# Kernel optimization log

Hardware: AMD Instinct MI355X
Metric: run time of the kernel (lower is better)

The kernel has to match this reference:

```python
import jax, jax.numpy as jnp
import numpy as np

B, S, D = 1, 2048, 2048
H, DH, DHID, DKER = 16, 128, 128, 64
EPS = 1e-6

def _gelu(x):
    return jax.nn.gelu(x, approximate=False)  # torch F.gelu default is exact erf

def setup_inputs() -> dict:
    key = jax.random.key(0)
    ks = jax.random.split(key, 12)
    inp = {
        'q': jax.random.normal(ks[0], (B, S, D), jnp.float32),
        'k': jax.random.normal(ks[1], (B, S, D), jnp.float32),
        'v': jax.random.normal(ks[2], (B, S, D), jnp.float32),
        'lr_attn_mask': jax.random.randint(ks[3], (1, 1, S, S), 0, 2) > 0,
        'sparse_norms_lse': jax.random.normal(ks[4], (B, H, S, 1), jnp.float32),
        'sparse_attn_weights': jax.random.normal(ks[5], (B, H, S, S), jnp.float32) * 0.1,
        'kernel_q_mat1': jax.random.normal(ks[6], (H, DH, DHID), jnp.float32) * 0.05,
        'kernel_k_mat1': jax.random.normal(ks[7], (H, DH, DHID), jnp.float32) * 0.05,
        'kernel_q_mat2': jax.random.normal(ks[8], (H, DHID, DKER), jnp.float32) * 0.05,
        'kernel_k_mat2': jax.random.normal(ks[9], (H, DHID, DKER), jnp.float32) * 0.05,
        'interaction_k': jax.random.normal(ks[10], (H, DKER, DKER), jnp.float32) * 0.05,
        'scalingD': jnp.ones((1, H, 1, DKER), jnp.float32) * 1e-4,
        'scalingD2': jnp.ones((1, H, 1, DKER), jnp.float32) * 1e-4,
    }
    return inp

def reference(q, k, v, lr_attn_mask, sparse_norms_lse, sparse_attn_weights,
              kernel_q_mat1, kernel_k_mat1, kernel_q_mat2, kernel_k_mat2,
              interaction_k, scalingD, scalingD2):
    b, s, d = q.shape
    dh = d // H
    # [B,S,D] -> [B,H,S,dh]
    q = q.reshape(b, s, H, dh).transpose(0, 2, 1, 3)
    k = k.reshape(b, s, H, dh).transpose(0, 2, 1, 3)
    v = v.reshape(b, s, H, dh).transpose(0, 2, 1, 3)
    # per-head kernel feature maps (dropout is identity, p=0.0)
    q = _gelu(jnp.einsum('bhsd,hde->bhse', q, kernel_q_mat1))
    q = _gelu(jnp.einsum('bhsd,hde->bhse', q, kernel_q_mat2))
    k = _gelu(jnp.einsum('bhsd,hde->bhse', k, kernel_k_mat1))
    k = jnp.abs(scalingD) * _gelu(jnp.einsum('bhsd,hde->bhse', k, kernel_k_mat2))
    k = k + jnp.einsum('bhse,hef->bhsf', k, interaction_k) * scalingD2
    # low-rank kernelized scores: [B,H,S,S]
    out = jnp.einsum('bhse,bhte->bhst', jnp.abs(q), jnp.abs(k))
    mask = lr_attn_mask  # bool, broadcasts over [B,H,S,S]
    out = jnp.where(mask, out, 0.0)
    lr_norms_lse = jnp.log(out.sum(axis=-1, keepdims=True) + EPS)
    norm_factor_lse = jnp.logaddexp(lr_norms_lse, sparse_norms_lse)
    # log-domain merge of low-rank and sparse scores
    out = jnp.where(mask, jnp.log(out + EPS), sparse_attn_weights)
    out = jnp.exp(out - norm_factor_lse)
    out = jnp.einsum('bhst,bhtd->bhsd', out, v)
    return out.transpose(0, 2, 1, 3).reshape(b, s, d)
```

## Files before the change

### kernel.cpp

```cpp
#include <hip/hip_runtime.h>
#include <math.h>

#define S 2048
#define DD 2048
#define NH 16
#define DH 128
#define DHID 128
#define DKER 64
#define EPSF 1e-6f

typedef __attribute__((ext_vector_type(8))) short bf16x8;
typedef __attribute__((ext_vector_type(4))) float f32x4;

__device__ __forceinline__ float gelu_f(float x) {
    return 0.5f * x * (1.0f + erff(x * 0.7071067811865475f));
}

__device__ __forceinline__ ushort f2b(float x) {
    uint32_t u = __float_as_uint(x);
    uint32_t r = (u + 0x7FFFu + ((u >> 16) & 1u)) >> 16;
    return (ushort)r;
}

__device__ __forceinline__ bf16x8 pack8(float4 a, float4 b) {
    bf16x8 r;
    r[0] = (short)f2b(a.x); r[1] = (short)f2b(a.y);
    r[2] = (short)f2b(a.z); r[3] = (short)f2b(a.w);
    r[4] = (short)f2b(b.x); r[5] = (short)f2b(b.y);
    r[6] = (short)f2b(b.z); r[7] = (short)f2b(b.w);
    return r;
}

__global__ __launch_bounds__(256) void k_wprep(const float* __restrict__ wq1,
                                               const float* __restrict__ wk1,
                                               const float* __restrict__ wq2,
                                               const float* __restrict__ wk2,
                                               const float* __restrict__ ik,
                                               ushort* __restrict__ w1qt,
                                               ushort* __restrict__ w1kt,
                                               ushort* __restrict__ w2qt,
                                               ushort* __restrict__ w2kt,
                                               ushort* __restrict__ ikt) {
    const int h = blockIdx.x, m = blockIdx.y, tid = threadIdx.x;
    const float* src; ushort* dst; int D;
    if (m == 0)      { src = wq1 + h * 16384; dst = w1qt + h * 16384; D = 128; }
    else if (m == 1) { src = wk1 + h * 16384; dst = w1kt + h * 16384; D = 128; }
    else if (m == 2) { src = wq2 + h * 8192;  dst = w2qt + h * 8192;  D = 128; }
    else if (m == 3) { src = wk2 + h * 8192;  dst = w2kt + h * 8192;  D = 128; }
    else             { src = ik  + h * 4096;  dst = ikt  + h * 4096;  D = 64;  }
    const int E = (m == 0 || m == 1) ? 128 : 64;
    const int dsh = (D == 128) ? 7 : 6;
    const int n = E * D;
    for (int idx = tid; idx < n; idx += 256) {
        int e = idx >> dsh, d = idx & (D - 1);
        dst[idx] = f2b(src[d * E + e]);
    }
}

__global__ __launch_bounds__(256) void k_fused(const float* __restrict__ Xq,
                                               const float* __restrict__ Xk,
                                               const ushort* __restrict__ w1qt,
                                               const ushort* __restrict__ w1kt,
                                               const ushort* __restrict__ w2qt,
                                               const ushort* __restrict__ w2kt,
                                               const ushort* __restrict__ ikt,
                                               const float* __restrict__ sD,
                                               const float* __restrict__ sD2,
                                               ushort* __restrict__ Q2,
                                               ushort* __restrict__ K3) {
    const int h = blockIdx.y;
    const int s0 = blockIdx.x * 64;
    const int z = blockIdx.z;
    const int tid = threadIdx.x;
    const int wv = tid >> 6, lane = tid & 63;
    const int ln = lane & 15, quad = lane >> 4;
    __shared__ ushort Y1s[64][136];
    __shared__ ushort K2s[64][72];

    const float* X = z ? Xk : Xq;
    const ushort* w1t = z ? w1kt : w1qt;
    const ushort* w2t = z ? w2kt : w2qt;

    const float* Xr = X + (size_t)(s0 + wv * 16 + ln) * DD + h * DH;
    bf16x8 a1[4];
    #pragma unroll
    for (int ks = 0; ks < 4; ++ks)
        a1[ks] = pack8(*(const float4*)(Xr + ks * 32 + quad * 8),
                       *(const float4*)(Xr + ks * 32 + quad * 8 + 4));

    const ushort* W1h = w1t + (size_t)h * DH * DHID;
    f32x4 c1[8];
    #pragma unroll
    for (int n = 0; n < 8; ++n) c1[n] = (f32x4){0.f, 0.f, 0.f, 0.f};
    #pragma unroll
    for (int n = 0; n < 8; ++n)
        #pragma unroll
        for (int ks = 0; ks < 4; ++ks) {
            bf16x8 b = *(const bf16x8*)(W1h + (size_t)(n * 16 + ln) * DHID +
                                        ks * 32 + quad * 8);
            c1[n] = __builtin_amdgcn_mfma_f32_16x16x32_bf16(a1[ks], b, c1[n], 0, 0, 0);
        }
    #pragma unroll
    for (int n = 0; n < 8; ++n)
        #pragma unroll
        for (int r = 0; r < 4; ++r)
            Y1s[wv * 16 + quad * 4 + r][n * 16 + ln] = f2b(gelu_f(c1[n][r]));

    bf16x8 a2[4];
    #pragma unroll
    for (int ks = 0; ks < 4; ++ks)
        a2[ks] = *(const bf16x8*)&Y1s[wv * 16 + ln][ks * 32 + quad * 8];
    const ushort* W2h = w2t + (size_t)h * DKER * DHID;
    f32x4 c2[4];
    #pragma unroll
    for (int n = 0; n < 4; ++n) c2[n] = (f32x4){0.f, 0.f, 0.f, 0.f};
    #pragma unroll
    for (int n = 0; n < 4; ++n)
        #pragma unroll
        for (int ks = 0; ks < 4; ++ks) {
            bf16x8 b = *(const bf16x8*)(W2h + (size_t)(n * 16 + ln) * DHID +
                                        ks * 32 + quad * 8);
            c2[n] = __builtin_amdgcn_mfma_f32_16x16x32_bf16(a2[ks], b, c2[n], 0, 0, 0);
        }

    if (z == 0) {
        #pragma unroll
        for (int n = 0; n < 4; ++n)
            #pragma unroll
            for (int r = 0; r < 4; ++r)
                Q2[((size_t)h * S + s0 + wv * 16 + quad * 4 + r) * DKER + n * 16 + ln] =
                    f2b(fabsf(gelu_f(c2[n][r])));
        return;
    }

    float k2v[4][4];
    float sdv[4], sd2v[4];
    #pragma unroll
    for (int n = 0; n < 4; ++n) {
        sdv[n]  = fabsf(sD[h * DKER + n * 16 + ln]);
        sd2v[n] = sD2[h * DKER + n * 16 + ln];
    }
    #pragma unroll
    for (int n = 0; n < 4; ++n)
        #pragma unroll
        for (int r = 0; r < 4; ++r) {
            k2v[n][r] = sdv[n] * gelu_f(c2[n][r]);
            K2s[wv * 16 + quad * 4 + r][n * 16 + ln] = f2b(k2v[n][r]);
        }
    bf16x8 a3[2];
    #pragma unroll
    for (int ks = 0; ks < 2; ++ks)
        a3[ks] = *(const bf16x8*)&K2s[wv * 16 + ln][ks * 32 + quad * 8];
    const ushort* Ikh = ikt + (size_t)h * DKER * DKER;
    f32x4 c3[4];
    #pragma unroll
    for (int n = 0; n < 4; ++n) c3[n] = (f32x4){0.f, 0.f, 0.f, 0.f};
    #pragma unroll
    for (int n = 0; n < 4; ++n)
        #pragma unroll
        for (int ks = 0; ks < 2; ++ks) {
            bf16x8 b = *(const bf16x8*)(Ikh + (size_t)(n * 16 + ln) * DKER +
                                        ks * 32 + quad * 8);
            c3[n] = __builtin_amdgcn_mfma_f32_16x16x32_bf16(a3[ks], b, c3[n], 0, 0, 0);
        }
    #pragma unroll
    for (int n = 0; n < 4; ++n)
        #pragma unroll
        for (int r = 0; r < 4; ++r)
            K3[((size_t)h * S + s0 + wv * 16 + quad * 4 + r) * DKER + n * 16 + ln] =
                f2b(fabsf(k2v[n][r] + c3[n][r] * sd2v[n]));
}

__global__ __launch_bounds__(256) void k_vt(const float* __restrict__ V,
                                            ushort* __restrict__ Vt) {
    const int h = blockIdx.y;
    const int t0 = blockIdx.x * 64;
    const int tid = threadIdx.x;
    __shared__ ushort Ls[128][72];
    #pragma unroll
    for (int it = 0; it < 8; ++it) {
        int idx = it * 256 + tid;
        int r = idx >> 5, c4 = idx & 31;
        float4 v = *(const float4*)(V + (size_t)(t0 + r) * DD + h * DH + c4 * 4);
        Ls[c4 * 4 + 0][r] = f2b(v.x);
        Ls[c4 * 4 + 1][r] = f2b(v.y);
        Ls[c4 * 4 + 2][r] = f2b(v.z);
        Ls[c4 * 4 + 3][r] = f2b(v.w);
    }
    __syncthreads();
    #pragma unroll
    for (int it = 0; it < 4; ++it) {
        int idx = it * 256 + tid;
        int row = idx >> 3, cc = idx & 7;
        *(bf16x8*)(Vt + ((size_t)h * DH + row) * S + t0 + cc * 8) =
            *(const bf16x8*)(&Ls[row][cc * 8]);
    }
}

__global__ __launch_bounds__(256) void k_mpack(const int* __restrict__ mask,
                                               uint* __restrict__ pm) {
    const int gw = blockIdx.x * 4 + (threadIdx.x >> 6);
    const int lane = threadIdx.x & 63;
    const int row = gw >> 5;
    const int w64 = gw & 31;
    int mv = mask[(size_t)row * S + w64 * 64 + lane];
    unsigned long long b = __ballot(mv != 0);
    if (lane == 0)  pm[row * 64 + w64 * 2]     = (uint)b;
    if (lane == 32) pm[row * 64 + w64 * 2 + 1] = (uint)(b >> 32);
}

__global__ __launch_bounds__(256, 2) void k_attn(const ushort* __restrict__ Q2,
                                                 const ushort* __restrict__ K3,
                                                 const ushort* __restrict__ Vt,
                                                 const uint* __restrict__ pm,
                                                 const float* __restrict__ Wsp,
                                                 const float* __restrict__ lse,
                                                 float* __restrict__ out) {
    const int h = blockIdx.y;
    const int s0 = blockIdx.x * 64;
    const int tid = threadIdx.x;
    const int wv = tid >> 6, lane = tid & 63;
    const int ln = lane & 15, quad = lane >> 4;
    __shared__ ushort K3s[64][72];
    __shared__ ushort Vts[128][72];
    __shared__ ushort Ps[4][16][72];

    const ushort* K3h = K3 + (size_t)h * S * DKER;
    const ushort* Vth = Vt + (size_t)h * DH * S;
    const float*  Wh  = Wsp + (size_t)h * S * S;
    const int srow_q = s0 + wv * 16 + quad * 4;
    const int rk = tid >> 3, ck = tid & 7;

    bf16x8 aq[2];
    #pragma unroll
    for (int ks = 0; ks < 2; ++ks)
        aq[ks] = *(const bf16x8*)(Q2 + ((size_t)h * S + s0 + wv * 16 + ln) * DKER +
                                  ks * 32 + quad * 8);

    f32x4 O[8];
    #pragma unroll
    for (int v = 0; v < 8; ++v) O[v] = (f32x4){0.f, 0.f, 0.f, 0.f};
    float rs[4] = {0.f, 0.f, 0.f, 0.f};

    bf16x8 sk[2][2], sv[2][4];
    float  ww[2][4][4];
    uint2  mw[2][4];

#define PREF(T, P) do {                                                            \
    if ((T) < 32) {                                                                \
        const int t0_ = (T) * 64;                                                  \
        _Pragma("unroll") for (int c_ = 0; c_ < 2; ++c_)                           \
            sk[P][c_] = *(const bf16x8*)(K3h +                                     \
                (size_t)(t0_ + rk + c_ * 32) * DKER + ck * 8);                     \
        _Pragma("unroll") for (int c_ = 0; c_ < 4; ++c_)                           \
            sv[P][c_] = *(const bf16x8*)(Vth +                                     \
                (size_t)(rk + c_ * 32) * S + t0_ + ck * 8);                        \
        _Pragma("unroll") for (int r_ = 0; r_ < 4; ++r_)                           \
            mw[P][r_] = *(const uint2*)(pm + (size_t)(srow_q + r_) * 64 +          \
                                        (t0_ >> 5));                               \
        _Pragma("unroll") for (int n_ = 0; n_ < 4; ++n_)                           \
        _Pragma("unroll") for (int r_ = 0; r_ < 4; ++r_)                           \
            ww[P][n_][r_] = Wh[(size_t)(srow_q + r_) * S + t0_ + n_ * 16 + ln];    \
    }                                                                              \
} while (0)

#define STEP(T, P, PN) do {                                                        \
    __syncthreads();                                 \
    _Pragma("unroll") for (int c_ = 0; c_ < 2; ++c_)                               \
        *(bf16x8*)&K3s[rk + c_ * 32][ck * 8] = sk[P][c_];                          \
    _Pragma("unroll") for (int c_ = 0; c_ < 4; ++c_)                               \
        *(bf16x8*)&Vts[rk + c_ * 32][ck * 8] = sv[P][c_];                          \
    __syncthreads();                                      \
    PREF((T) + 1, PN);      \
    f32x4 sc[4];                                                                   \
    _Pragma("unroll") for (int n_ = 0; n_ < 4; ++n_)                               \
        sc[n_] = (f32x4){0.f, 0.f, 0.f, 0.f};                                      \
    _Pragma("unroll") for (int ks_ = 0; ks_ < 2; ++ks_)                            \
    _Pragma("unroll") for (int n_ = 0; n_ < 4; ++n_) {                             \
        bf16x8 bf = *(const bf16x8*)&K3s[n_ * 16 + ln][ks_ * 32 + quad * 8];       \
        sc[n_] = __builtin_amdgcn_mfma_f32_16x16x32_bf16(aq[ks_], bf, sc[n_],      \
                                                         0, 0, 0);                  \
    }                                                                              \
    _Pragma("unroll") for (int n_ = 0; n_ < 4; ++n_)                               \
    _Pragma("unroll") for (int r_ = 0; r_ < 4; ++r_) {                             \
        uint word = (n_ >= 2) ? mw[P][r_].y : mw[P][r_].x;                         \
        int m_ = (word >> (((n_ & 1) << 4) + ln)) & 1;                             \
        float s_ = sc[n_][r_];                                                     \
        float p_;                                                                  \
        if (m_) { rs[r_] += s_; p_ = s_ + EPSF; }                                  \
        else    { p_ = __expf(ww[P][n_][r_]); }                                    \
        Ps[wv][quad * 4 + r_][n_ * 16 + ln] = f2b(p_);                             \
    }                                                                              \
    _Pragma("unroll") for (int ks_ = 0; ks_ < 2; ++ks_) {                          \
        bf16x8 pf = *(const bf16x8*)&Ps[wv][ln][ks_ * 32 + quad * 8];              \
        _Pragma("unroll") for (int v_ = 0; v_ < 8; ++v_) {                         \
            bf16x8 vf = *(const bf16x8*)&Vts[v_ * 16 + ln][ks_ * 32 + quad * 8];   \
            O[v_] = __builtin_amdgcn_mfma_f32_16x16x32_bf16(pf, vf, O[v_],         \
                                                            0, 0, 0);               \
        }                                                                          \
    }                                                                              \
} while (0)

    PREF(0, 0);
    for (int it = 0; it < 32; it += 2) {
        STEP(it, 0, 1);
        STEP(it + 1, 1, 0);
    }
#undef PREF
#undef STEP

    #pragma unroll
    for (int r = 0; r < 4; ++r) {
        float v = rs[r];
        v += __shfl_xor(v, 1); v += __shfl_xor(v, 2);
        v += __shfl_xor(v, 4); v += __shfl_xor(v, 8);
        rs[r] = v;
    }
    float idv[4];
    #pragma unroll
    for (int r = 0; r < 4; ++r)
        idv[r] = 1.f / (rs[r] + EPSF + expf(lse[(size_t)h * S + srow_q + r]));
    #pragma unroll
    for (int v = 0; v < 8; ++v)
        #pragma unroll
        for (int r = 0; r < 4; ++r)
            out[(size_t)(srow_q + r) * DD + h * DH + v * 16 + ln] = O[v][r] * idv[r];
}

extern "C" void kernel_launch(void* const* d_in, const int* in_sizes, int n_in,
                              void* d_out, int out_size, void* d_ws, size_t ws_size,
                              hipStream_t stream) {
    const float* q   = (const float*)d_in[0];
    const float* k   = (const float*)d_in[1];
    const float* v   = (const float*)d_in[2];
    const int*   msk = (const int*)d_in[3];
    const float* lse = (const float*)d_in[4];
    const float* spw = (const float*)d_in[5];
    const float* wq1 = (const float*)d_in[6];
    const float* wk1 = (const float*)d_in[7];
    const float* wq2 = (const float*)d_in[8];
    const float* wk2 = (const float*)d_in[9];
    const float* ik  = (const float*)d_in[10];
    const float* sD  = (const float*)d_in[11];
    const float* sD2 = (const float*)d_in[12];
    float* out = (float*)d_out;

    ushort* q2b  = (ushort*)d_ws;
    ushort* k3b  = q2b + (size_t)NH * S * DKER;
    ushort* vt   = k3b + (size_t)NH * S * DKER;
    uint*   pm   = (uint*)(vt + (size_t)NH * DH * S);
    ushort* w1qt = (ushort*)(pm + (size_t)S * 64);
    ushort* w1kt = w1qt + (size_t)NH * DH * DHID;
    ushort* w2qt = w1kt + (size_t)NH * DH * DHID;
    ushort* w2kt = w2qt + (size_t)NH * DKER * DHID;
    ushort* ikt  = w2kt + (size_t)NH * DKER * DHID;

    dim3 g(S / 64, NH), b(256);
    k_wprep<<<dim3(NH, 5), b, 0, stream>>>(wq1, wk1, wq2, wk2, ik,
                                           w1qt, w1kt, w2qt, w2kt, ikt);
    k_mpack<<<dim3(S * 32 / 4), b, 0, stream>>>(msk, pm);
    k_vt<<<g, b, 0, stream>>>(v, vt);
    k_fused<<<dim3(S / 64, NH, 2), b, 0, stream>>>(q, k, w1qt, w1kt, w2qt, w2kt,
                                                   ikt, sD, sD2, q2b, k3b);
    k_attn<<<g, b, 0, stream>>>(q2b, k3b, vt, pm, spw, lse, out);
}
```

Before: 495.2 us.

## Split sparse exp(W)·V into separate streaming kernel and simplify attention loop

Adds a k_ev kernel that streams the large sparse weight tensor with vector float4 loads. It applies exp or EPS according to the mask bits and multiplies by V with MFMA, writing a per-head partial output EV. k_attn then only computes the masked low-rank scores times V, adds EV in the epilogue, and no longer reads the sparse weights. K and V are read directly from global memory instead of being staged through LDS, and both kernels use a swizzled 1D block index with higher occupancy bounds. This decouples the bandwidth-heavy sparse stream from the MFMA-heavy path, at the cost of an extra fp32 intermediate write and read and of reading V twice.

Result: slower. 746.9 us (+50.8%).

```diff
diff --git a/kernel.cpp b/kernel.cpp
--- a/kernel.cpp
+++ b/kernel.cpp
@@ -209,32 +209,87 @@
     if (lane == 32) pm[row * 64 + w64 * 2 + 1] = (uint)(b >> 32);
 }
 
-__global__ __launch_bounds__(256, 2) void k_attn(const ushort* __restrict__ Q2,
+__global__ __launch_bounds__(256, 4) void k_ev(const float* __restrict__ Wsp,
+                                               const ushort* __restrict__ Vt,
+                                               const uint* __restrict__ pm,
+                                               float* __restrict__ EV) {
+    const int bid = blockIdx.x;
+    const int id = (bid & 7) * 64 + (bid >> 3);
+    const int h = id >> 5;
+    const int s0 = (id & 31) * 64;
+    const int tid = threadIdx.x;
+    const int wv = tid >> 6, lane = tid & 63;
+    const int ln = lane & 15, quad = lane >> 4;
+    const int arow = s0 + wv * 16 + ln;
+
+    const float*  Wr  = Wsp + (size_t)h * S * S + (size_t)arow * S;
+    const uint*   pr  = pm + (size_t)arow * 64;
+    const ushort* Vth = Vt + (size_t)h * DH * S;
+
+    f32x4 O[8];
+    #pragma unroll
+    for (int v = 0; v < 8; ++v) O[v] = (f32x4){0.f, 0.f, 0.f, 0.f};
+
+    for (int t0 = 0; t0 < S; t0 += 64) {
+        uint2 mword = *(const uint2*)(pr + (t0 >> 5));
+        bf16x8 a[2];
+        #pragma unroll
+        for (int ks = 0; ks < 2; ++ks) {
+            const float* wp = Wr + t0 + ks * 32 + quad * 8;
+            float4 w0 = *(const float4*)wp;
+            float4 w1 = *(const float4*)(wp + 4);
+            uint mb = (ks ? mword.y : mword.x) >> (quad * 8);
+            float p[8];
+            p[0] = w0.x; p[1] = w0.y; p[2] = w0.z; p[3] = w0.w;
+            p[4] = w1.x; p[5] = w1.y; p[6] = w1.z; p[7] = w1.w;
+            #pragma unroll
+            for (int j = 0; j < 8; ++j)
+                p[j] = ((mb >> j) & 1) ? EPSF : __expf(p[j]);
+            a[ks] = pack8(make_float4(p[0], p[1], p[2], p[3]),
+                          make_float4(p[4], p[5], p[6], p[7]));
+        }
+        #pragma unroll
+        for (int ks = 0; ks < 2; ++ks)
+            #pragma unroll
+            for (int v = 0; v < 8; ++v) {
+                bf16x8 vf = *(const bf16x8*)(Vth + (size_t)(v * 16 + ln) * S +
+                                             t0 + ks * 32 + quad * 8);
+                O[v] = __builtin_amdgcn_mfma_f32_16x16x32_bf16(a[ks], vf, O[v], 0, 0, 0);
+            }
+    }
+    const int orow = s0 + wv * 16 + quad * 4;
+    #pragma unroll
+    for (int v = 0; v < 8; ++v)
+        #pragma unroll
+        for (int r = 0; r < 4; ++r)
+            EV[((size_t)h * S + orow + r) * DH + v * 16 + ln] = O[v][r];
+}
+
+__global__ __launch_bounds__(256, 3) void k_attn(const ushort* __restrict__ Q2,
                                                  const ushort* __restrict__ K3,
                                                  const ushort* __restrict__ Vt,
                                                  const uint* __restrict__ pm,
-                                                 const float* __restrict__ Wsp,
+                                                 const float* __restrict__ EV,
                                                  const float* __restrict__ lse,
                                                  float* __restrict__ out) {
-    const int h = blockIdx.y;
-    const int s0 = blockIdx.x * 64;
+    const int bid = blockIdx.x;
+    const int id = (bid & 7) * 64 + (bid >> 3);
+    const int h = id >> 5;
+    const int s0 = (id & 31) * 64;
     const int tid = threadIdx.x;
     const int wv = tid >> 6, lane = tid & 63;
     const int ln = lane & 15, quad = lane >> 4;
-    __shared__ ushort K3s[64][72];
-    __shared__ ushort Vts[128][72];
     __shared__ ushort Ps[4][16][72];
 
     const ushort* K3h = K3 + (size_t)h * S * DKER;
     const ushort* Vth = Vt + (size_t)h * DH * S;
-    const float*  Wh  = Wsp + (size_t)h * S * S;
     const int srow_q = s0 + wv * 16 + quad * 4;
-    const int rk = tid >> 3, ck = tid & 7;
+    const int arow = s0 + wv * 16 + ln;
 
     bf16x8 aq[2];
     #pragma unroll
     for (int ks = 0; ks < 2; ++ks)
-        aq[ks] = *(const bf16x8*)(Q2 + ((size_t)h * S + s0 + wv * 16 + ln) * DKER +
+        aq[ks] = *(const bf16x8*)(Q2 + ((size_t)h * S + arow) * DKER +
                                   ks * 32 + quad * 8);
 
     f32x4 O[8];
@@ -242,72 +297,47 @@
     for (int v = 0; v < 8; ++v) O[v] = (f32x4){0.f, 0.f, 0.f, 0.f};
     float rs[4] = {0.f, 0.f, 0.f, 0.f};
 
-    bf16x8 sk[2][2], sv[2][4];
-    float  ww[2][4][4];
-    uint2  mw[2][4];
-
-#define PREF(T, P) do {                                                            \
-    if ((T) < 32) {                                                                \
-        const int t0_ = (T) * 64;                                                  \
-        _Pragma("unroll") for (int c_ = 0; c_ < 2; ++c_)                           \
-            sk[P][c_] = *(const bf16x8*)(K3h +                                     \
-                (size_t)(t0_ + rk + c_ * 32) * DKER + ck * 8);                     \
-        _Pragma("unroll") for (int c_ = 0; c_ < 4; ++c_)                           \
-            sv[P][c_] = *(const bf16x8*)(Vth +                                     \
-                (size_t)(rk + c_ * 32) * S + t0_ + ck * 8);                        \
-        _Pragma("unroll") for (int r_ = 0; r_ < 4; ++r_)                           \
-            mw[P][r_] = *(const uint2*)(pm + (size_t)(srow_q + r_) * 64 +          \
-                                        (t0_ >> 5));                               \
-        _Pragma("unroll") for (int n_ = 0; n_ < 4; ++n_)                           \
-        _Pragma("unroll") for (int r_ = 0; r_ < 4; ++r_)                           \
-            ww[P][n_][r_] = Wh[(size_t)(srow_q + r_) * S + t0_ + n_ * 16 + ln];    \
-    }                                                                              \
-} while (0)
-
-#define STEP(T, P, PN) do {                                                        \
-    __syncthreads();                                 \
-    _Pragma("unroll") for (int c_ = 0; c_ < 2; ++c_)                               \
-        *(bf16x8*)&K3s[rk + c_ * 32][ck * 8] = sk[P][c_];                          \
-    _Pragma("unroll") for (int c_ = 0; c_ < 4; ++c_)                               \
-        *(bf16x8*)&Vts[rk + c_ * 32][ck * 8] = sv[P][c_];                          \
-    __syncthreads();                                      \
-    PREF((T) + 1, PN);      \
-    f32x4 sc[4];                                                                   \
-    _Pragma("unroll") for (int n_ = 0; n_ < 4; ++n_)                               \
-        sc[n_] = (f32x4){0.f, 0.f, 0.f, 0.f};                                      \
-    _Pragma("unroll") for (int ks_ = 0; ks_ < 2; ++ks_)                            \
-    _Pragma("unroll") for (int n_ = 0; n_ < 4; ++n_) {                             \
-        bf16x8 bf = *(const bf16x8*)&K3s[n_ * 16 + ln][ks_ * 32 + quad * 8];       \
-        sc[n_] = __builtin_amdgcn_mfma_f32_16x16x32_bf16(aq[ks_], bf, sc[n_],      \
-                                                         0, 0, 0);                  \
-    }                                                                              \
-    _Pragma("unroll") for (int n_ = 0; n_ < 4; ++n_)                               \
-    _Pragma("unroll") for (int r_ = 0; r_ < 4; ++r_) {                             \
-        uint word = (n_ >= 2) ? mw[P][r_].y : mw[P][r_].x;                         \
-        int m_ = (word >> (((n_ & 1) << 4) + ln)) & 1;                             \
-        float s_ = sc[n_][r_];                                                     \
-        float p_;                                                                  \
-        if (m_) { rs[r_] += s_; p_ = s_ + EPSF; }                                  \
-        else    { p_ = __expf(ww[P][n_][r_]); }                                    \
-        Ps[wv][quad * 4 + r_][n_ * 16 + ln] = f2b(p_);                             \
-    }                                                                              \
-    _Pragma("unroll") for (int ks_ = 0; ks_ < 2; ++ks_) {                          \
-        bf16x8 pf = *(const bf16x8*)&Ps[wv][ln][ks_ * 32 + quad * 8];              \
-        _Pragma("unroll") for (int v_ = 0; v_ < 8; ++v_) {                         \
-            bf16x8 vf = *(const bf16x8*)&Vts[v_ * 16 + ln][ks_ * 32 + quad * 8];   \
-            O[v_] = __builtin_amdgcn_mfma_f32_16x16x32_bf16(pf, vf, O[v_],         \
-                                                            0, 0, 0);               \
-        }                                                                          \
-    }                                                                              \
-} while (0)
-
-    PREF(0, 0);
-    for (int it = 0; it < 32; it += 2) {
-        STEP(it, 0, 1);
-        STEP(it + 1, 1, 0);
-    }
-#undef PREF
-#undef STEP
+    for (int t0 = 0; t0 < S; t0 += 64) {
+        uint2 mw[4];
+        #pragma unroll
+        for (int r = 0; r < 4; ++r)
+            mw[r] = *(const uint2*)(pm + (size_t)(srow_q + r) * 64 + (t0 >> 5));
+
+        f32x4 sc[4];
+        #pragma unroll
+        for (int n = 0; n < 4; ++n) sc[n] = (f32x4){0.f, 0.f, 0.f, 0.f};
+        #pragma unroll
+        for (int ks = 0; ks < 2; ++ks)
+            #pragma unroll
+            for (int n = 0; n < 4; ++n) {
+                bf16x8 bf = *(const bf16x8*)(K3h + (size_t)(t0 + n * 16 + ln) * DKER +
+                                             ks * 32 + quad * 8);
+                sc[n] = __builtin_amdgcn_mfma_f32_16x16x32_bf16(aq[ks], bf, sc[n], 0, 0, 0);
+            }
+
+        #pragma unroll
+        for (int n = 0; n < 4; ++n)
+            #pragma unroll
+            for (int r = 0; r < 4; ++r) {
+                uint word = (n >= 2) ? mw[r].y : mw[r].x;
+                int m = (word >> (((n & 1) << 4) + ln)) & 1;
+                float s = sc[n][r];
+                float p = m ? s : 0.f;
+                rs[r] += p;
+                Ps[wv][quad * 4 + r][n * 16 + ln] = f2b(p);
+            }
+
+        #pragma unroll
+        for (int ks = 0; ks < 2; ++ks) {
+            bf16x8 pf = *(const bf16x8*)&Ps[wv][ln][ks * 32 + quad * 8];
+            #pragma unroll
+            for (int v = 0; v < 8; ++v) {
+                bf16x8 vf = *(const bf16x8*)(Vth + (size_t)(v * 16 + ln) * S +
+                                             t0 + ks * 32 + quad * 8);
+                O[v] = __builtin_amdgcn_mfma_f32_16x16x32_bf16(pf, vf, O[v], 0, 0, 0);
+            }
+        }
+    }
 
     #pragma unroll
     for (int r = 0; r < 4; ++r) {
@@ -320,11 +350,13 @@
     #pragma unroll
     for (int r = 0; r < 4; ++r)
         idv[r] = 1.f / (rs[r] + EPSF + expf(lse[(size_t)h * S + srow_q + r]));
+    const float* EVh = EV + ((size_t)h * S + srow_q) * DH;
     #pragma unroll
     for (int v = 0; v < 8; ++v)
         #pragma unroll
         for (int r = 0; r < 4; ++r)
-            out[(size_t)(srow_q + r) * DD + h * DH + v * 16 + ln] = O[v][r] * idv[r];
+            out[(size_t)(srow_q + r) * DD + h * DH + v * 16 + ln] =
+                (O[v][r] + EVh[r * DH + v * 16 + ln]) * idv[r];
 }
 
 extern "C" void kernel_launch(void* const* d_in, const int* in_sizes, int n_in,
@@ -354,6 +386,7 @@
     ushort* w2qt = w1kt + (size_t)NH * DH * DHID;
     ushort* w2kt = w2qt + (size_t)NH * DKER * DHID;
     ushort* ikt  = w2kt + (size_t)NH * DKER * DHID;
+    float*  ev   = (float*)(ikt + (size_t)NH * DKER * DKER);
 
     dim3 g(S / 64, NH), b(256);
     k_wprep<<<dim3(NH, 5), b, 0, stream>>>(wq1, wk1, wq2, wk2, ik,
@@ -362,5 +395,6 @@
     k_vt<<<g, b, 0, stream>>>(v, vt);
     k_fused<<<dim3(S / 64, NH, 2), b, 0, stream>>>(q, k, w1qt, w1kt, w2qt, w2kt,
                                                    ikt, sD, sD2, q2b, k3b);
-    k_attn<<<g, b, 0, stream>>>(q2b, k3b, vt, pm, spw, lse, out);
-}
+    k_ev<<<dim3(512), b, 0, stream>>>(spw, vt, pm, ev);
+    k_attn<<<dim3(512), b, 0, stream>>>(q2b, k3b, vt, pm, ev, lse, out);
+}
```

## Vectorize sparse-weight loads in A-fragment layout and remap attention blocks

Applied to the files above, without the earlier changes.

The attention kernel now loads the sparse attention weights as float4 rows that match the MFMA A-operand layout, two tiles ahead. The masked/sparse merge is applied after reading the score tile back from LDS, which replaces 16 scalar strided loads per tile with coalesced vector loads. Attention blocks are launched on a 1-D grid remapped so that consecutive blocks come from different heads, spreading them across XCDs/L2. The feature-map GEMM loops are also reordered to batch the weight-fragment loads ahead of the MFMAs. In exchange, scores are rounded to bf16 before the EPS add, and more registers are held for the prefetch buffers.

New measurement: 501.7 us. About the same (+1.3%).

```diff
diff --git a/kernel.cpp b/kernel.cpp
--- a/kernel.cpp
+++ b/kernel.cpp
@@ -29,6 +29,18 @@
     r[4] = (short)f2b(b.x); r[5] = (short)f2b(b.y);
     r[6] = (short)f2b(b.z); r[7] = (short)f2b(b.w);
     return r;
+}
+
+__device__ __forceinline__ bf16x8 merge8(bf16x8 ps, uint mb, float4 wa, float4 wb) {
+    float w[8] = {wa.x, wa.y, wa.z, wa.w, wb.x, wb.y, wb.z, wb.w};
+    float p[8];
+    #pragma unroll
+    for (int j = 0; j < 8; ++j) {
+        float sv = __uint_as_float(((uint)(ushort)ps[j]) << 16);
+        p[j] = ((mb >> j) & 1) ? (sv + EPSF) : __expf(w[j]);
+    }
+    return pack8(make_float4(p[0], p[1], p[2], p[3]),
+                 make_float4(p[4], p[5], p[6], p[7]));
 }
 
 __global__ __launch_bounds__(256) void k_wprep(const float* __restrict__ wq1,
@@ -93,13 +105,16 @@
     #pragma unroll
     for (int n = 0; n < 8; ++n) c1[n] = (f32x4){0.f, 0.f, 0.f, 0.f};
     #pragma unroll
-    for (int n = 0; n < 8; ++n)
-        #pragma unroll
-        for (int ks = 0; ks < 4; ++ks) {
-            bf16x8 b = *(const bf16x8*)(W1h + (size_t)(n * 16 + ln) * DHID +
-                                        ks * 32 + quad * 8);
-            c1[n] = __builtin_amdgcn_mfma_f32_16x16x32_bf16(a1[ks], b, c1[n], 0, 0, 0);
-        }
+    for (int ks = 0; ks < 4; ++ks) {
+        bf16x8 bb[8];
+        #pragma unroll
+        for (int n = 0; n < 8; ++n)
+            bb[n] = *(const bf16x8*)(W1h + (size_t)(n * 16 + ln) * DHID +
+                                     ks * 32 + quad * 8);
+        #pragma unroll
+        for (int n = 0; n < 8; ++n)
+            c1[n] = __builtin_amdgcn_mfma_f32_16x16x32_bf16(a1[ks], bb[n], c1[n], 0, 0, 0);
+    }
     #pragma unroll
     for (int n = 0; n < 8; ++n)
         #pragma unroll
@@ -115,13 +130,16 @@
     #pragma unroll
     for (int n = 0; n < 4; ++n) c2[n] = (f32x4){0.f, 0.f, 0.f, 0.f};
     #pragma unroll
-    for (int n = 0; n < 4; ++n)
-        #pragma unroll
-        for (int ks = 0; ks < 4; ++ks) {
-            bf16x8 b = *(const bf16x8*)(W2h + (size_t)(n * 16 + ln) * DHID +
-                                        ks * 32 + quad * 8);
-            c2[n] = __builtin_amdgcn_mfma_f32_16x16x32_bf16(a2[ks], b, c2[n], 0, 0, 0);
-        }
+    for (int ks = 0; ks < 4; ++ks) {
+        bf16x8 bb[4];
+        #pragma unroll
+        for (int n = 0; n < 4; ++n)
+            bb[n] = *(const bf16x8*)(W2h + (size_t)(n * 16 + ln) * DHID +
+                                     ks * 32 + quad * 8);
+        #pragma unroll
+        for (int n = 0; n < 4; ++n)
+            c2[n] = __builtin_amdgcn_mfma_f32_16x16x32_bf16(a2[ks], bb[n], c2[n], 0, 0, 0);
+    }
 
     if (z == 0) {
         #pragma unroll
@@ -156,13 +174,16 @@
     #pragma unroll
     for (int n = 0; n < 4; ++n) c3[n] = (f32x4){0.f, 0.f, 0.f, 0.f};
     #pragma unroll
-    for (int n = 0; n < 4; ++n)
-        #pragma unroll
-        for (int ks = 0; ks < 2; ++ks) {
-            bf16x8 b = *(const bf16x8*)(Ikh + (size_t)(n * 16 + ln) * DKER +
-                                        ks * 32 + quad * 8);
-            c3[n] = __builtin_amdgcn_mfma_f32_16x16x32_bf16(a3[ks], b, c3[n], 0, 0, 0);
-        }
+    for (int ks = 0; ks < 2; ++ks) {
+        bf16x8 bb[4];
+        #pragma unroll
+        for (int n = 0; n < 4; ++n)
+            bb[n] = *(const bf16x8*)(Ikh + (size_t)(n * 16 + ln) * DKER +
+                                     ks * 32 + quad * 8);
+        #pragma unroll
+        for (int n = 0; n < 4; ++n)
+            c3[n] = __builtin_amdgcn_mfma_f32_16x16x32_bf16(a3[ks], bb[n], c3[n], 0, 0, 0);
+    }
     #pragma unroll
     for (int n = 0; n < 4; ++n)
         #pragma unroll
@@ -216,8 +237,10 @@
                                                  const float* __restrict__ Wsp,
                                                  const float* __restrict__ lse,
                                                  float* __restrict__ out) {
-    const int h = blockIdx.y;
-    const int s0 = blockIdx.x * 64;
+    const int bid = blockIdx.x;
+    const int id = (bid & 7) * 64 + (bid >> 3);
+    const int h = id >> 5;
+    const int s0 = (id & 31) * 64;
     const int tid = threadIdx.x;
     const int wv = tid >> 6, lane = tid & 63;
     const int ln = lane & 15, quad = lane >> 4;
@@ -227,14 +250,17 @@
 
     const ushort* K3h = K3 + (size_t)h * S * DKER;
     const ushort* Vth = Vt + (size_t)h * DH * S;
-    const float*  Wh  = Wsp + (size_t)h * S * S;
     const int srow_q = s0 + wv * 16 + quad * 4;
+    const int arow   = s0 + wv * 16 + ln;
     const int rk = tid >> 3, ck = tid & 7;
 
+    const float* Wr = Wsp + (size_t)h * S * S + (size_t)arow * S;
+    const uint*  pr = pm + (size_t)arow * 64;
+
     bf16x8 aq[2];
     #pragma unroll
     for (int ks = 0; ks < 2; ++ks)
-        aq[ks] = *(const bf16x8*)(Q2 + ((size_t)h * S + s0 + wv * 16 + ln) * DKER +
+        aq[ks] = *(const bf16x8*)(Q2 + ((size_t)h * S + arow) * DKER +
                                   ks * 32 + quad * 8);
 
     f32x4 O[8];
@@ -243,10 +269,22 @@
     float rs[4] = {0.f, 0.f, 0.f, 0.f};
 
     bf16x8 sk[2][2], sv[2][4];
-    float  ww[2][4][4];
     uint2  mw[2][4];
-
-#define PREF(T, P) do {                                                            \
+    float4 wbuf[2][4];
+    uint2  mwa[2];
+
+#define PREF_W(T, SL) do {                                                         \
+    if ((T) < 32) {                                                                \
+        const float* wp_ = Wr + (T) * 64 + quad * 8;                               \
+        wbuf[SL][0] = *(const float4*)wp_;                                         \
+        wbuf[SL][1] = *(const float4*)(wp_ + 4);                                   \
+        wbuf[SL][2] = *(const float4*)(wp_ + 32);                                  \
+        wbuf[SL][3] = *(const float4*)(wp_ + 36);                                  \
+        mwa[SL] = *(const uint2*)(pr + (T) * 2);                                   \
+    }                                                                              \
+} while (0)
+
+#define PREF_KV(T, P) do {                                                         \
     if ((T) < 32) {                                                                \
         const int t0_ = (T) * 64;                                                  \
         _Pragma("unroll") for (int c_ = 0; c_ < 2; ++c_)                           \
@@ -257,10 +295,7 @@
                 (size_t)(rk + c_ * 32) * S + t0_ + ck * 8);                        \
         _Pragma("unroll") for (int r_ = 0; r_ < 4; ++r_)                           \
             mw[P][r_] = *(const uint2*)(pm + (size_t)(srow_q + r_) * 64 +          \
-                                        (t0_ >> 5));                               \
-        _Pragma("unroll") for (int n_ = 0; n_ < 4; ++n_)                           \
-        _Pragma("unroll") for (int r_ = 0; r_ < 4; ++r_)                           \
-            ww[P][n_][r_] = Wh[(size_t)(srow_q + r_) * S + t0_ + n_ * 16 + ln];    \
+                                        (T) * 2);                                  \
     }                                                                              \
 } while (0)
 
@@ -271,7 +306,7 @@
     _Pragma("unroll") for (int c_ = 0; c_ < 4; ++c_)                               \
         *(bf16x8*)&Vts[rk + c_ * 32][ck * 8] = sv[P][c_];                          \
     __syncthreads();                                      \
-    PREF((T) + 1, PN);      \
+    PREF_KV((T) + 1, PN);                                                          \
     f32x4 sc[4];                                                                   \
     _Pragma("unroll") for (int n_ = 0; n_ < 4; ++n_)                               \
         sc[n_] = (f32x4){0.f, 0.f, 0.f, 0.f};                                      \
@@ -286,27 +321,40 @@
         uint word = (n_ >= 2) ? mw[P][r_].y : mw[P][r_].x;                         \
         int m_ = (word >> (((n_ & 1) << 4) + ln)) & 1;                             \
         float s_ = sc[n_][r_];                                                     \
-        float p_;                                                                  \
-        if (m_) { rs[r_] += s_; p_ = s_ + EPSF; }                                  \
-        else    { p_ = __expf(ww[P][n_][r_]); }                                    \
-        Ps[wv][quad * 4 + r_][n_ * 16 + ln] = f2b(p_);                             \
-    }                                                                              \
-    _Pragma("unroll") for (int ks_ = 0; ks_ < 2; ++ks_) {                          \
-        bf16x8 pf = *(const bf16x8*)&Ps[wv][ln][ks_ * 32 + quad * 8];              \
-        _Pragma("unroll") for (int v_ = 0; v_ < 8; ++v_) {                         \
-            bf16x8 vf = *(const bf16x8*)&Vts[v_ * 16 + ln][ks_ * 32 + quad * 8];   \
-            O[v_] = __builtin_amdgcn_mfma_f32_16x16x32_bf16(pf, vf, O[v_],         \
-                                                            0, 0, 0);               \
-        }                                                                          \
+        if (m_) rs[r_] += s_;                                                      \
+        Ps[wv][quad * 4 + r_][n_ * 16 + ln] = f2b(s_);                             \
+    }                                                                              \
+                \
+    bf16x8 pa0, pa1;                                                               \
+    {                                                                              \
+        bf16x8 ps0 = *(const bf16x8*)&Ps[wv][ln][quad * 8];                        \
+        bf16x8 ps1 = *(const bf16x8*)&Ps[wv][ln][32 + quad * 8];                   \
+        uint2 ma_ = mwa[(T) & 1];                                                  \
+        pa0 = merge8(ps0, ma_.x >> (quad * 8), wbuf[(T) & 1][0],                   \
+                     wbuf[(T) & 1][1]);                                            \
+        pa1 = merge8(ps1, ma_.y >> (quad * 8), wbuf[(T) & 1][2],                   \
+                     wbuf[(T) & 1][3]);                                            \
+    }                                                                              \
+    PREF_W((T) + 2, (T) & 1);                   \
+    _Pragma("unroll") for (int v_ = 0; v_ < 8; ++v_) {                             \
+        bf16x8 vf = *(const bf16x8*)&Vts[v_ * 16 + ln][quad * 8];                  \
+        O[v_] = __builtin_amdgcn_mfma_f32_16x16x32_bf16(pa0, vf, O[v_], 0, 0, 0);  \
+    }                                                                              \
+    _Pragma("unroll") for (int v_ = 0; v_ < 8; ++v_) {                             \
+        bf16x8 vf = *(const bf16x8*)&Vts[v_ * 16 + ln][32 + quad * 8];             \
+        O[v_] = __builtin_amdgcn_mfma_f32_16x16x32_bf16(pa1, vf, O[v_], 0, 0, 0);  \
     }                                                                              \
 } while (0)
 
-    PREF(0, 0);
+    PREF_W(0, 0);
+    PREF_W(1, 1);
+    PREF_KV(0, 0);
     for (int it = 0; it < 32; it += 2) {
         STEP(it, 0, 1);
         STEP(it + 1, 1, 0);
     }
-#undef PREF
+#undef PREF_W
+#undef PREF_KV
 #undef STEP
 
     #pragma unroll
@@ -362,5 +410,5 @@
     k_vt<<<g, b, 0, stream>>>(v, vt);
     k_fused<<<dim3(S / 64, NH, 2), b, 0, stream>>>(q, k, w1qt, w1kt, w2qt, w2kt,
                                                    ikt, sD, sD2, q2b, k3b);
-    k_attn<<<g, b, 0, stream>>>(q2b, k3b, vt, pm, spw, lse, out);
-}
+    k_attn<<<dim3(512), b, 0, stream>>>(q2b, k3b, vt, pm, spw, lse, out);
+}
```
